# Performance work log

Hardware: AMD Instinct MI355X
Metric: run time of the kernel (lower is better)

## Reference

```python
import jax, jax.numpy as jnp
import numpy as np

EDGE_DROPOUT = 0.1   # init kwarg edge_dropout
TRAINING = True      # init kwarg is_training
N_NODES = 8192
D_FEAT = 512


def setup_inputs() -> dict:
    key = jax.random.key(0)
    x = jax.random.normal(key, (N_NODES, D_FEAT), dtype=jnp.float32)
    return {"x": x, "k": 30}


def _graph_process(x, k):
    # knn_fast: cosine similarity kNN with symmetric degree normalization.
    n = x.shape[0]
    xn = x / jnp.linalg.norm(x, axis=1, keepdims=True)      # F.normalize(x, dim=1)
    sim = xn @ xn.T                                         # [n, n] (torch does this in blocks of 1000; same math)
    vals, inds = jax.lax.top_k(sim, k + 1)                  # [n, k+1]
    rows = jnp.broadcast_to(jnp.arange(n)[:, None], vals.shape).reshape(-1)
    cols = inds.reshape(-1)
    v = vals.reshape(-1)
    norm_row = vals.sum(axis=1)                             # out-degree mass
    norm_col = jnp.zeros(n, vals.dtype).at[cols].add(v)     # in-degree mass (index_add_)
    norm = norm_row + norm_col
    v = v * (norm[rows] ** -0.5) * (norm[cols] ** -0.5)
    # values[torch.isnan(values)] = 0
    v = jnp.where(jnp.isnan(v), jnp.zeros_like(v), v)
    # symmetrize edge list
    rows_ = jnp.concatenate([rows, cols])
    cols_ = jnp.concatenate([cols, rows])
    v_ = jnp.concatenate([v, v])
    v_ = jax.nn.relu(v_)
    if TRAINING and EDGE_DROPOUT > 0.0:
        keep = jax.random.bernoulli(jax.random.key(42), 1.0 - EDGE_DROPOUT, v_.shape)
        v_ = jnp.where(keep, v_ / (1.0 - EDGE_DROPOUT), jnp.zeros_like(v_))
    # sparse_coo_tensor(...).coalesce(): duplicate (i,j) entries sum -> dense scatter-add
    adj = jnp.zeros((n, n), v_.dtype).at[rows_, cols_].add(v_)
    return adj


def reference(x, k):
    return _graph_process(x, k)
```

## Files before the change

kernel.cpp:

```cpp
#include <hip/hip_runtime.h>
#include <cstdint>
#include <cmath>

#define NN 8192
#define DD 512
#define KP1 31
#define HALF_EDGES (NN * KP1)

__device__ __forceinline__ uint32_t rotl32(uint32_t v, int s) {
  return (v << s) | (v >> (32 - s));
}

__device__ __forceinline__ void threefry2x32_42(uint32_t x0, uint32_t x1,
                                                uint32_t& o0, uint32_t& o1) {
  const uint32_t ks0 = 0u, ks1 = 42u;
  const uint32_t ks2 = 0x1BD11BDAu ^ ks0 ^ ks1;
  x0 += ks0; x1 += ks1;
  x0 += x1; x1 = rotl32(x1, 13); x1 ^= x0;
  x0 += x1; x1 = rotl32(x1, 15); x1 ^= x0;
  x0 += x1; x1 = rotl32(x1, 26); x1 ^= x0;
  x0 += x1; x1 = rotl32(x1, 6);  x1 ^= x0;
  x0 += ks1; x1 += ks2 + 1u;
  x0 += x1; x1 = rotl32(x1, 17); x1 ^= x0;
  x0 += x1; x1 = rotl32(x1, 29); x1 ^= x0;
  x0 += x1; x1 = rotl32(x1, 16); x1 ^= x0;
  x0 += x1; x1 = rotl32(x1, 24); x1 ^= x0;
  x0 += ks2; x1 += ks0 + 2u;
  x0 += x1; x1 = rotl32(x1, 13); x1 ^= x0;
  x0 += x1; x1 = rotl32(x1, 15); x1 ^= x0;
  x0 += x1; x1 = rotl32(x1, 26); x1 ^= x0;
  x0 += x1; x1 = rotl32(x1, 6);  x1 ^= x0;
  x0 += ks0; x1 += ks1 + 3u;
  x0 += x1; x1 = rotl32(x1, 17); x1 ^= x0;
  x0 += x1; x1 = rotl32(x1, 29); x1 ^= x0;
  x0 += x1; x1 = rotl32(x1, 16); x1 ^= x0;
  x0 += x1; x1 = rotl32(x1, 24); x1 ^= x0;
  x0 += ks1; x1 += ks2 + 4u;
  x0 += x1; x1 = rotl32(x1, 13); x1 ^= x0;
  x0 += x1; x1 = rotl32(x1, 15); x1 ^= x0;
  x0 += x1; x1 = rotl32(x1, 26); x1 ^= x0;
  x0 += x1; x1 = rotl32(x1, 6);  x1 ^= x0;
  x0 += ks2; x1 += ks0 + 5u;
  o0 = x0; o1 = x1;
}

__device__ __forceinline__ bool keep_edge(uint32_t e) {
  uint32_t y0, y1;
  threefry2x32_42(0u, e, y0, y1);
  uint32_t bits = y0 ^ y1;
  float u = __uint_as_float((bits >> 9) | 0x3f800000u) - 1.0f;
  return u < 0.9f;
}

__global__ __launch_bounds__(256) void rownorm_kernel(const float* __restrict__ x,
                                                      float* __restrict__ nrm) {
#pragma clang fp contract(off)
  __shared__ float rowbuf[16][DD];
  __shared__ float partial[16][4];
  int tid = threadIdx.x;
  int rowbase = blockIdx.x * 16;

  for (int p = 0; p < 8; ++p) {
    int f = tid + p * 256;
    int r = f >> 7, k4 = f & 127;
    *(float4*)(&rowbuf[r][k4 << 2]) =
        *(const float4*)(x + (size_t)(rowbase + r) * DD + (k4 << 2));
  }
  __syncthreads();
  if (tid < 64) {
    int r = tid >> 2, q = tid & 3;
    const float* s = &rowbuf[r][q * 128];
    float a0 = s[0]*s[0], a1 = s[1]*s[1], a2 = s[2]*s[2], a3 = s[3]*s[3];
    float a4 = s[4]*s[4], a5 = s[5]*s[5], a6 = s[6]*s[6], a7 = s[7]*s[7];
    for (int i = 8; i < 128; i += 8) {
      a0 += s[i+0]*s[i+0]; a1 += s[i+1]*s[i+1];
      a2 += s[i+2]*s[i+2]; a3 += s[i+3]*s[i+3];
      a4 += s[i+4]*s[i+4]; a5 += s[i+5]*s[i+5];
      a6 += s[i+6]*s[i+6]; a7 += s[i+7]*s[i+7];
    }
    partial[r][q] = ((a0 + a1) + (a2 + a3)) + ((a4 + a5) + (a6 + a7));
  }
  __syncthreads();
  if (tid < 16) {
    float S = (partial[tid][0] + partial[tid][1]) + (partial[tid][2] + partial[tid][3]);
    nrm[rowbase + tid] = sqrtf(S);
  }
}

__global__ __launch_bounds__(256, 2) void gemm_kernel(const float* __restrict__ x,
                                                      const float* __restrict__ nrm,
                                                      float* __restrict__ out) {
#pragma clang fp contract(off)
  int bid = blockIdx.x;
  int by = (int)((129.0f - sqrtf(16641.0f - 8.0f * (float)bid)) * 0.5f);
  while (64 * by - (by * (by - 1)) / 2 > bid) --by;
  while (64 * (by + 1) - ((by + 1) * by) / 2 <= bid) ++by;
  const int bx = by + (bid - (64 * by - (by * (by - 1)) / 2));

  extern __shared__ char smem[];
  float4* AsF4 = (float4*)smem;
  float4* BsF4 = (float4*)(smem + 32768);

  const int tid = threadIdx.x;
  const int rb = by * 128;
  const int cb = bx * 128;
  const int m = tid & 15;
  const int g = tid >> 4;

  float nA[8], nB[8];
  #pragma unroll
  for (int p = 0; p < 8; ++p) {
    nA[p] = nrm[rb + g + 16 * p];
    nB[p] = nrm[cb + g + 16 * p];
  }

  const int lane = tid & 63, wave = tid >> 6;
  const int wr = wave >> 1, wc = wave & 1;
  const int lr = lane >> 3, lc = lane & 7;
  const int r0 = wr * 64 + lr * 8;
  const int c0 = wc * 64 + lc;
  const int rsw = r0 >> 3;

  float acc[8][8];
  #pragma unroll
  for (int i = 0; i < 8; ++i)
    #pragma unroll
    for (int j = 0; j < 8; ++j) acc[i][j] = 0.f;

  const float4* xv = (const float4*)x;

  float4 ra[8], rbv[8];
  #pragma unroll
  for (int p = 0; p < 8; ++p) {
    int r = g + 16 * p;
    ra[p]  = xv[(size_t)(rb + r) * 128 + m];
    rbv[p] = xv[(size_t)(cb + r) * 128 + m];
  }

  for (int kc = 0; kc < 8; ++kc) {
    __syncthreads();
    #pragma unroll
    for (int p = 0; p < 8; ++p) {
      int r = g + 16 * p;
      float4 va = ra[p];
      va.x = va.x / nA[p]; va.y = va.y / nA[p];
      va.z = va.z / nA[p]; va.w = va.w / nA[p];
      AsF4[r * 16 + ((m + (r >> 3)) & 15)] = va;
      float4 vb = rbv[p];
      vb.x = vb.x / nB[p]; vb.y = vb.y / nB[p];
      vb.z = vb.z / nB[p]; vb.w = vb.w / nB[p];
      BsF4[r * 16 + ((m + r) & 15)] = vb;
    }
    __syncthreads();
    if (kc < 7) {
      #pragma unroll
      for (int p = 0; p < 8; ++p) {
        int r = g + 16 * p;
        ra[p]  = xv[(size_t)(rb + r) * 128 + (kc + 1) * 16 + m];
        rbv[p] = xv[(size_t)(cb + r) * 128 + (kc + 1) * 16 + m];
      }
    }

    #pragma unroll 2
    for (int k4 = 0; k4 < 16; ++k4) {
      float4 av[8], bv[8];
      int tA = (k4 + rsw) & 15;
      #pragma unroll
      for (int i = 0; i < 8; ++i) av[i] = AsF4[(r0 + i) * 16 + tA];
      #pragma unroll
      for (int j = 0; j < 8; ++j)
        bv[j] = BsF4[(c0 + 8 * j) * 16 + ((k4 + lc + 8 * j) & 15)];
      #pragma unroll
      for (int kk = 0; kk < 4; ++kk) {
        #pragma unroll
        for (int i = 0; i < 8; ++i) {
          float a = ((const float*)&av[i])[kk];
          #pragma unroll
          for (int j = 0; j < 8; ++j) {
            float b = ((const float*)&bv[j])[kk];
            acc[i][j] = acc[i][j] + a * b;
          }
        }
      }
    }
  }

  float* Cs = (float*)smem;
  float4* outv = (float4*)out;
  const bool offdiag = (rb != cb);
  for (int half = 0; half < 2; ++half) {
    __syncthreads();
    if (wr == half) {
      #pragma unroll
      for (int i = 0; i < 8; ++i)
        #pragma unroll
        for (int j = 0; j < 8; ++j)
          Cs[(lr * 8 + i) * 129 + wc * 64 + 8 * j + lc] = acc[i][j];
    }
    __syncthreads();
    #pragma unroll
    for (int q = 0; q < 8; ++q) {
      int f2 = tid + q * 256;
      int rl = f2 >> 5, c4 = f2 & 31;
      float4 o;
      o.x = Cs[rl * 129 + 4 * c4 + 0];
      o.y = Cs[rl * 129 + 4 * c4 + 1];
      o.z = Cs[rl * 129 + 4 * c4 + 2];
      o.w = Cs[rl * 129 + 4 * c4 + 3];
      outv[(size_t)(rb + half * 64 + rl) * 2048 + (cb >> 2) + c4] = o;
    }
    if (offdiag) {
      #pragma unroll
      for (int q = 0; q < 8; ++q) {
        int f2 = tid + q * 256;
        int c = f2 >> 4, t4 = f2 & 15;
        float4 o;
        o.x = Cs[(4 * t4 + 0) * 129 + c];
        o.y = Cs[(4 * t4 + 1) * 129 + c];
        o.z = Cs[(4 * t4 + 2) * 129 + c];
        o.w = Cs[(4 * t4 + 3) * 129 + c];
        outv[(size_t)(cb + c) * 2048 + ((rb + half * 64) >> 2) + t4] = o;
      }
    }
  }
}

__global__ __launch_bounds__(256) void topk_kernel(const float* __restrict__ sim,
                                                   float* __restrict__ vals,
                                                   int* __restrict__ inds) {
  const int w = threadIdx.x >> 6;
  const int lane = threadIdx.x & 63;
  const int row = blockIdx.x * 4 + w;

  float kval = -1e30f;
  int   kidx = 0;
  float kmin = -1e30f;

  const float* srow = sim + (size_t)row * NN;
  for (int grp = 0; grp < NN / 64; ++grp) {
    float v = srow[grp * 64 + lane];
    unsigned long long mask = __ballot(v > kmin);
    while (mask) {
      int src = __builtin_ctzll(mask);
      mask &= mask - 1;
      float vv = __shfl(v, src, 64);
      if (vv > kmin) {
        int cc = grp * 64 + src;
        unsigned long long ge = __ballot(kval >= vv) & 0x7FFFFFFFull;
        int pos = __popcll(ge);
        float upv = __shfl_up(kval, 1, 64);
        int   upi = __shfl_up(kidx, 1, 64);
        if (lane < KP1) {
          if (lane == pos) { kval = vv; kidx = cc; }
          else if (lane > pos) { kval = upv; kidx = upi; }
        }
        kmin = __shfl(kval, KP1 - 1, 64);
      }
    }
  }
  if (lane < KP1) {
    vals[(size_t)row * KP1 + lane] = kval;
    inds[row * KP1 + lane] = kidx;
  }
}

__global__ __launch_bounds__(256) void norm_kernel(const float* __restrict__ vals,
                                                   const int* __restrict__ inds,
                                                   float* __restrict__ norm) {
  int i = blockIdx.x * blockDim.x + threadIdx.x;
  if (i >= NN) return;
  float s = 0.f;
  for (int t = 0; t < KP1; ++t) {
    float v = vals[i * KP1 + t];
    s += v;
    atomicAdd(&norm[inds[i * KP1 + t]], v);
  }
  atomicAdd(&norm[i], s);
}

__global__ __launch_bounds__(256) void scatter_kernel(const float* __restrict__ vals,
                                                      const int* __restrict__ inds,
                                                      const float* __restrict__ norm,
                                                      float* __restrict__ out) {
  int e = blockIdx.x * blockDim.x + threadIdx.x;
  if (e >= HALF_EDGES) return;
  int i = e / KP1;
  int c = inds[e];
  float v = vals[e];
  float nv = v * (1.0f / sqrtf(norm[i])) * (1.0f / sqrtf(norm[c]));
  if (isnan(nv)) nv = 0.f;
  nv = fmaxf(nv, 0.f);
  float scaled = nv / 0.9f;
  if (keep_edge((uint32_t)e))
    atomicAdd(out + (size_t)i * NN + c, scaled);
  if (keep_edge((uint32_t)(e + HALF_EDGES)))
    atomicAdd(out + (size_t)c * NN + i, scaled);
}

extern "C" void kernel_launch(void* const* d_in, const int* in_sizes, int n_in,
                              void* d_out, int out_size, void* d_ws, size_t ws_size,
                              hipStream_t stream) {
  (void)in_sizes; (void)n_in; (void)ws_size;
  const float* x = (const float*)d_in[0];
  float* out = (float*)d_out;

  float* nrm  = (float*)d_ws;
  float* vals = nrm + NN;
  int*   inds = (int*)(vals + HALF_EDGES);
  float* norm = (float*)(inds + HALF_EDGES);

  hipLaunchKernelGGL(rownorm_kernel, dim3(NN / 16), dim3(256), 0, stream, x, nrm);
  hipLaunchKernelGGL(gemm_kernel, dim3(2080), dim3(256), 65536, stream,
                     x, nrm, out);
  hipLaunchKernelGGL(topk_kernel, dim3(NN / 4), dim3(256), 0, stream,
                     out, vals, inds);
  hipMemsetAsync(norm, 0, NN * sizeof(float), stream);
  hipLaunchKernelGGL(norm_kernel, dim3((NN + 255) / 256), dim3(256), 0, stream,
                     vals, inds, norm);
  hipMemsetAsync(d_out, 0, (size_t)out_size * sizeof(float), stream);
  hipLaunchKernelGGL(scatter_kernel, dim3((HALF_EDGES + 255) / 256), dim3(256), 0, stream,
                     vals, inds, norm, out);
}
```

Before: 1.288 ms.

## Restructure similarity GEMM with packed FMA, k-major B tile, and prenormalized input

Adds a separate pass that writes normalized x into workspace so the GEMM no longer divides on every tile load, with a fallback when the workspace is too small. The GEMM k-chunk is halved to cut shared memory from 64KB to 32KB, and B is stored k-major with an XOR swizzle so each thread reads contiguous float4 columns. Accumulation uses 2-wide float vectors, which may lower to packed FP32 FMA. The direct tile is written straight from registers, and the transposed mirror goes through a smaller staged buffer. The cost is an extra full pass over x and more synchronisation rounds in the mirror write.

```diff
diff --git a/kernel.cpp b/kernel.cpp
--- a/kernel.cpp
+++ b/kernel.cpp
@@ -6,6 +6,8 @@
 #define DD 512
 #define KP1 31
 #define HALF_EDGES (NN * KP1)
+
+typedef float f2 __attribute__((ext_vector_type(2)));
 
 __device__ __forceinline__ uint32_t rotl32(uint32_t v, int s) {
   return (v << s) | (v >> (32 - s));
@@ -87,6 +89,20 @@
   }
 }
 
+__global__ __launch_bounds__(256) void xnorm_kernel(const float* __restrict__ x,
+                                                    const float* __restrict__ nrm,
+                                                    float* __restrict__ xn) {
+#pragma clang fp contract(off)
+  int idx = blockIdx.x * 256 + threadIdx.x;
+  const float4* xv = (const float4*)x;
+  float4* xo = (float4*)xn;
+  float4 v = xv[idx];
+  float n = nrm[idx >> 7];
+  v.x = v.x / n; v.y = v.y / n; v.z = v.z / n; v.w = v.w / n;
+  xo[idx] = v;
+}
+
+template <bool PRE>
 __global__ __launch_bounds__(256, 2) void gemm_kernel(const float* __restrict__ x,
                                                       const float* __restrict__ nrm,
                                                       float* __restrict__ out) {
@@ -99,127 +115,147 @@
 
   extern __shared__ char smem[];
   float4* AsF4 = (float4*)smem;
-  float4* BsF4 = (float4*)(smem + 32768);
+  float*  Bs   = (float*)(smem + 16384);
 
   const int tid = threadIdx.x;
   const int rb = by * 128;
   const int cb = bx * 128;
-  const int m = tid & 15;
-  const int g = tid >> 4;
-
-  float nA[8], nB[8];
-  #pragma unroll
-  for (int p = 0; p < 8; ++p) {
-    nA[p] = nrm[rb + g + 16 * p];
-    nB[p] = nrm[cb + g + 16 * p];
+  const int m = tid & 7;
+  const int g = tid >> 3;
+
+  float nA[4], nB[4];
+  if (!PRE) {
+    #pragma unroll
+    for (int p = 0; p < 4; ++p) {
+      nA[p] = nrm[rb + g + 32 * p];
+      nB[p] = nrm[cb + g + 32 * p];
+    }
   }
 
   const int lane = tid & 63, wave = tid >> 6;
   const int wr = wave >> 1, wc = wave & 1;
   const int lr = lane >> 3, lc = lane & 7;
   const int r0 = wr * 64 + lr * 8;
-  const int c0 = wc * 64 + lc;
-  const int rsw = r0 >> 3;
-
-  float acc[8][8];
+  const int c0 = wc * 64 + lc * 8;
+
+  f2 acc[8][4];
   #pragma unroll
   for (int i = 0; i < 8; ++i)
     #pragma unroll
-    for (int j = 0; j < 8; ++j) acc[i][j] = 0.f;
+    for (int jp = 0; jp < 4; ++jp) { acc[i][jp].x = 0.f; acc[i][jp].y = 0.f; }
 
   const float4* xv = (const float4*)x;
 
-  float4 ra[8], rbv[8];
+  float4 ra[4], rbv[4];
   #pragma unroll
-  for (int p = 0; p < 8; ++p) {
-    int r = g + 16 * p;
+  for (int p = 0; p < 4; ++p) {
+    int r = g + 32 * p;
     ra[p]  = xv[(size_t)(rb + r) * 128 + m];
     rbv[p] = xv[(size_t)(cb + r) * 128 + m];
   }
 
-  for (int kc = 0; kc < 8; ++kc) {
+  for (int kc = 0; kc < 16; ++kc) {
     __syncthreads();
     #pragma unroll
-    for (int p = 0; p < 8; ++p) {
-      int r = g + 16 * p;
+    for (int p = 0; p < 4; ++p) {
+      int r = g + 32 * p;
       float4 va = ra[p];
-      va.x = va.x / nA[p]; va.y = va.y / nA[p];
-      va.z = va.z / nA[p]; va.w = va.w / nA[p];
-      AsF4[r * 16 + ((m + (r >> 3)) & 15)] = va;
+      if (!PRE) {
+        va.x = va.x / nA[p]; va.y = va.y / nA[p];
+        va.z = va.z / nA[p]; va.w = va.w / nA[p];
+      }
+      AsF4[r * 8 + ((m + (r >> 3)) & 7)] = va;
       float4 vb = rbv[p];
-      vb.x = vb.x / nB[p]; vb.y = vb.y / nB[p];
-      vb.z = vb.z / nB[p]; vb.w = vb.w / nB[p];
-      BsF4[r * 16 + ((m + r) & 15)] = vb;
+      if (!PRE) {
+        vb.x = vb.x / nB[p]; vb.y = vb.y / nB[p];
+        vb.z = vb.z / nB[p]; vb.w = vb.w / nB[p];
+      }
+      float* bp = Bs + (4 * m) * 128 + (r ^ ((m & 3) << 3));
+      bp[0]   = vb.x;
+      bp[128] = vb.y;
+      bp[256] = vb.z;
+      bp[384] = vb.w;
     }
     __syncthreads();
-    if (kc < 7) {
-      #pragma unroll
-      for (int p = 0; p < 8; ++p) {
-        int r = g + 16 * p;
-        ra[p]  = xv[(size_t)(rb + r) * 128 + (kc + 1) * 16 + m];
-        rbv[p] = xv[(size_t)(cb + r) * 128 + (kc + 1) * 16 + m];
+    if (kc < 15) {
+      #pragma unroll
+      for (int p = 0; p < 4; ++p) {
+        int r = g + 32 * p;
+        ra[p]  = xv[(size_t)(rb + r) * 128 + (kc + 1) * 8 + m];
+        rbv[p] = xv[(size_t)(cb + r) * 128 + (kc + 1) * 8 + m];
       }
     }
 
     #pragma unroll 2
-    for (int k4 = 0; k4 < 16; ++k4) {
-      float4 av[8], bv[8];
-      int tA = (k4 + rsw) & 15;
-      #pragma unroll
-      for (int i = 0; i < 8; ++i) av[i] = AsF4[(r0 + i) * 16 + tA];
-      #pragma unroll
-      for (int j = 0; j < 8; ++j)
-        bv[j] = BsF4[(c0 + 8 * j) * 16 + ((k4 + lc + 8 * j) & 15)];
+    for (int k4 = 0; k4 < 8; ++k4) {
+      float4 av[8];
+      const int tA = (k4 + (r0 >> 3)) & 7;
+      #pragma unroll
+      for (int i = 0; i < 8; ++i) av[i] = AsF4[(r0 + i) * 8 + tA];
+      float4 b01[8];
+      const int csw = c0 ^ ((k4 & 3) << 3);
       #pragma unroll
       for (int kk = 0; kk < 4; ++kk) {
+        const float* bp = Bs + (4 * k4 + kk) * 128 + csw;
+        b01[2 * kk]     = *(const float4*)(bp);
+        b01[2 * kk + 1] = *(const float4*)(bp + 4);
+      }
+      #pragma unroll
+      for (int kk = 0; kk < 4; ++kk) {
+        f2 bb0 = {b01[2 * kk].x,     b01[2 * kk].y};
+        f2 bb1 = {b01[2 * kk].z,     b01[2 * kk].w};
+        f2 bb2 = {b01[2 * kk + 1].x, b01[2 * kk + 1].y};
+        f2 bb3 = {b01[2 * kk + 1].z, b01[2 * kk + 1].w};
         #pragma unroll
         for (int i = 0; i < 8; ++i) {
           float a = ((const float*)&av[i])[kk];
+          f2 t0 = a * bb0; acc[i][0] = acc[i][0] + t0;
+          f2 t1 = a * bb1; acc[i][1] = acc[i][1] + t1;
+          f2 t2 = a * bb2; acc[i][2] = acc[i][2] + t2;
+          f2 t3 = a * bb3; acc[i][3] = acc[i][3] + t3;
+        }
+      }
+    }
+  }
+
+  float4* outv = (float4*)out;
+
+  #pragma unroll
+  for (int i = 0; i < 8; ++i) {
+    #pragma unroll
+    for (int h = 0; h < 2; ++h) {
+      float4 o;
+      o.x = acc[i][2 * h].x;     o.y = acc[i][2 * h].y;
+      o.z = acc[i][2 * h + 1].x; o.w = acc[i][2 * h + 1].y;
+      outv[(size_t)(rb + r0 + i) * 2048 + ((cb + c0) >> 2) + h] = o;
+    }
+  }
+
+  if (rb != cb) {
+    float* Cs = (float*)smem;
+    #pragma unroll 1
+    for (int q = 0; q < 4; ++q) {
+      __syncthreads();
+      if (wr == (q >> 1) && (lr >> 2) == (q & 1)) {
+        const int rB = (lr & 3) * 8;
+        #pragma unroll
+        for (int i = 0; i < 8; ++i) {
           #pragma unroll
-          for (int j = 0; j < 8; ++j) {
-            float b = ((const float*)&bv[j])[kk];
-            acc[i][j] = acc[i][j] + a * b;
-          }
+          for (int jp = 0; jp < 4; ++jp)
+            *(f2*)(Cs + (rB + i) * 130 + wc * 64 + lc * 8 + 2 * jp) = acc[i][jp];
         }
       }
-    }
-  }
-
-  float* Cs = (float*)smem;
-  float4* outv = (float4*)out;
-  const bool offdiag = (rb != cb);
-  for (int half = 0; half < 2; ++half) {
-    __syncthreads();
-    if (wr == half) {
-      #pragma unroll
-      for (int i = 0; i < 8; ++i)
-        #pragma unroll
-        for (int j = 0; j < 8; ++j)
-          Cs[(lr * 8 + i) * 129 + wc * 64 + 8 * j + lc] = acc[i][j];
-    }
-    __syncthreads();
-    #pragma unroll
-    for (int q = 0; q < 8; ++q) {
-      int f2 = tid + q * 256;
-      int rl = f2 >> 5, c4 = f2 & 31;
-      float4 o;
-      o.x = Cs[rl * 129 + 4 * c4 + 0];
-      o.y = Cs[rl * 129 + 4 * c4 + 1];
-      o.z = Cs[rl * 129 + 4 * c4 + 2];
-      o.w = Cs[rl * 129 + 4 * c4 + 3];
-      outv[(size_t)(rb + half * 64 + rl) * 2048 + (cb >> 2) + c4] = o;
-    }
-    if (offdiag) {
-      #pragma unroll
-      for (int q = 0; q < 8; ++q) {
-        int f2 = tid + q * 256;
-        int c = f2 >> 4, t4 = f2 & 15;
+      __syncthreads();
+      #pragma unroll
+      for (int q2 = 0; q2 < 4; ++q2) {
+        int f = tid + q2 * 256;
+        int c = f >> 3, t4 = f & 7;
         float4 o;
-        o.x = Cs[(4 * t4 + 0) * 129 + c];
-        o.y = Cs[(4 * t4 + 1) * 129 + c];
-        o.z = Cs[(4 * t4 + 2) * 129 + c];
-        o.w = Cs[(4 * t4 + 3) * 129 + c];
-        outv[(size_t)(cb + c) * 2048 + ((rb + half * 64) >> 2) + t4] = o;
+        o.x = Cs[(4 * t4 + 0) * 130 + c];
+        o.y = Cs[(4 * t4 + 1) * 130 + c];
+        o.z = Cs[(4 * t4 + 2) * 130 + c];
+        o.w = Cs[(4 * t4 + 3) * 130 + c];
+        outv[(size_t)(cb + c) * 2048 + ((rb + q * 32) >> 2) + t4] = o;
       }
     }
   }
@@ -300,7 +336,7 @@
 extern "C" void kernel_launch(void* const* d_in, const int* in_sizes, int n_in,
                               void* d_out, int out_size, void* d_ws, size_t ws_size,
                               hipStream_t stream) {
-  (void)in_sizes; (void)n_in; (void)ws_size;
+  (void)in_sizes; (void)n_in;
   const float* x = (const float*)d_in[0];
   float* out = (float*)d_out;
 
@@ -308,10 +344,19 @@
   float* vals = nrm + NN;
   int*   inds = (int*)(vals + HALF_EDGES);
   float* norm = (float*)(inds + HALF_EDGES);
+  float* xn   = (float*)((char*)d_ws + (size_t)(2 * 1024 * 1024));
+  const bool pre = ws_size >= (size_t)(2 * 1024 * 1024) + (size_t)NN * DD * 4;
 
   hipLaunchKernelGGL(rownorm_kernel, dim3(NN / 16), dim3(256), 0, stream, x, nrm);
-  hipLaunchKernelGGL(gemm_kernel, dim3(2080), dim3(256), 65536, stream,
-                     x, nrm, out);
+  if (pre) {
+    hipLaunchKernelGGL(xnorm_kernel, dim3(NN * DD / 4 / 256), dim3(256), 0, stream,
+                       x, nrm, xn);
+    hipLaunchKernelGGL((gemm_kernel<true>), dim3(2080), dim3(256), 32768, stream,
+                       xn, (const float*)nullptr, out);
+  } else {
+    hipLaunchKernelGGL((gemm_kernel<false>), dim3(2080), dim3(256), 32768, stream,
+                       x, nrm, out);
+  }
   hipLaunchKernelGGL(topk_kernel, dim3(NN / 4), dim3(256), 0, stream,
                      out, vals, inds);
   hipMemsetAsync(norm, 0, NN * sizeof(float), stream);
```

Measured after the change: 1.103 ms. -14.4%, faster.
